# Performance work log

Hardware: AMD Instinct MI355X
Metric: run time of the kernel (lower is better)

## Reference

```python
import jax, jax.numpy as jnp
import numpy as np

HIDDEN = 1024
OUT = 16

def setup_inputs() -> dict:
    key = jax.random.key(0)
    ks = jax.random.split(key, 12)
    bs, hl, hf = 256, 256, 32
    T, ad = 64, 16
    flat = hl * hf
    s = lambda fi, fo: 1.0 / np.sqrt(fi)
    return {
        "history": jax.random.normal(ks[0], (bs, hl, hf), jnp.float32),
        "action": jax.random.normal(ks[1], (bs, T, ad), jnp.float32),
        # carry-init Dense layers (c and h)
        "Wc": jax.random.normal(ks[2], (flat, HIDDEN), jnp.float32) * s(flat, HIDDEN),
        "bc": jnp.zeros((HIDDEN,), jnp.float32),
        "Wh": jax.random.normal(ks[3], (flat, HIDDEN), jnp.float32) * s(flat, HIDDEN),
        "bh": jnp.zeros((HIDDEN,), jnp.float32),
        # LSTM cell: gates ordered [i, f, g, o]; input dense has no bias (flax LSTMCell)
        "Wi": jax.random.normal(ks[4], (ad, 4 * HIDDEN), jnp.float32) * s(ad, HIDDEN),
        "Wr": jax.random.normal(ks[5], (HIDDEN, 4 * HIDDEN), jnp.float32) * s(HIDDEN, HIDDEN),
        "bg": jnp.zeros((4 * HIDDEN,), jnp.float32),
        # output projection
        "Wo": jax.random.normal(ks[6], (HIDDEN, OUT), jnp.float32) * s(HIDDEN, OUT),
        "bo": jnp.zeros((OUT,), jnp.float32),
    }


def reference(history, action, Wc, bc, Wh, bh, Wi, Wr, bg, Wo, bo):
    bs = history.shape[0]
    flat = history.reshape(bs, -1)
    c0 = jax.nn.relu(flat @ Wc + bc)  # [bs, H]
    h0 = jax.nn.relu(flat @ Wh + bh)  # [bs, H]

    # precompute input contribution to gates for all steps: [T, bs, 4H]
    xg = jnp.einsum('bta,ag->tbg', action, Wi)

    def step(carry, xg_t):
        c, h = carry
        g = xg_t + h @ Wr + bg  # [bs, 4H]
        i, f, gg, o = jnp.split(g, 4, axis=-1)
        c = jax.nn.sigmoid(f) * c + jax.nn.sigmoid(i) * jnp.tanh(gg)
        h = jax.nn.sigmoid(o) * jnp.tanh(c)
        return (c, h), h

    _, hs = jax.lax.scan(step, (c0, h0), xg)  # hs: [T, bs, H]
    x = jnp.transpose(hs, (1, 0, 2))  # [bs, T, H]
    # Dropout is deterministic (identity)
    return x @ Wo + bo  # [bs, T, OUT]
```

## Files before the change

### kernel.cpp

```cpp
#include <hip/hip_runtime.h>
#include <math.h>

#define BS      256
#define FLAT    8192
#define H       1024
#define G4      4096
#define T_STEPS 64
#define AD      16
#define NOUT    16

typedef __attribute__((ext_vector_type(8))) short    bf16x8;
typedef __attribute__((ext_vector_type(4))) float    f32x4;
typedef __attribute__((ext_vector_type(8))) unsigned short u16x8;

__device__ __forceinline__ float sigf(float x) { return 1.0f / (1.0f + __expf(-x)); }
__device__ __forceinline__ float tanh_fast(float x) {
    float a = fabsf(x);
    float e = __expf(-2.0f * a);
    float r = (1.0f - e) / (1.0f + e);
    return copysignf(r, x);
}
__device__ __forceinline__ unsigned short f2bf(float x) {
    unsigned int u = __float_as_uint(x);
    unsigned int r = (u + 0x7FFFu + ((u >> 16) & 1u)) >> 16;
    return (unsigned short)r;
}

#define OFF_WRP  (1u<<20)
#define OFF_WIP  (OFF_WRP + (8u<<20))
#define OFF_BGP  (OFF_WIP + (256u<<10))
#define OFF_WOP  (OFF_BGP + (16u<<10))
#define OFF_BAR  (OFF_WOP + (32u<<10))
#define OFF_AXP  (10u<<20)
#define OFF_HALL (11u<<20)
#define OFF_AHP  (44u<<20)
#define OFF_PART (48u<<20)

#define HALL_STRIDE 262144u

__global__ __launch_bounds__(256) void pack_wr(const float* __restrict__ Wr,
                                               unsigned short* __restrict__ Wp)
{
    int g  = blockIdx.x * 256 + threadIdx.x;
    int l  = g & 63;
    int nt = (g >> 6) & 3;
    int kc = (g >> 8) & 31;
    int nb = g >> 13;
    int col   = nt * 1024 + nb * 16 + (l & 15);
    int kbase = kc * 32 + (l >> 4) * 8;
    u16x8 o;
    #pragma unroll
    for (int i = 0; i < 8; ++i)
        o[i] = f2bf(Wr[(size_t)(kbase + i) * G4 + col]);
    *(u16x8*)&Wp[(size_t)g * 8] = o;
}

__global__ __launch_bounds__(256) void pack_wi(const float* __restrict__ Wi,
                                               unsigned short* __restrict__ Wp)
{
    int g  = blockIdx.x * 256 + threadIdx.x;
    int l  = g & 63;
    int nt = (g >> 6) & 3;
    int nb = g >> 8;
    int col   = nt * 1024 + nb * 16 + (l & 15);
    int kbase = (l >> 4) * 8;
    u16x8 o;
    #pragma unroll
    for (int i = 0; i < 8; ++i)
        o[i] = (kbase + i < AD) ? f2bf(Wi[(size_t)(kbase + i) * G4 + col]) : (unsigned short)0;
    *(u16x8*)&Wp[(size_t)g * 8] = o;
}

__global__ __launch_bounds__(256) void pack_bg(const float* __restrict__ bg,
                                               float* __restrict__ bgp)
{
    int t = blockIdx.x * 256 + threadIdx.x;
    int jj = t & 15, nt = (t >> 4) & 3, nb = t >> 6;
    bgp[t] = bg[nt * 1024 + nb * 16 + jj];
}

__global__ __launch_bounds__(256) void pack_hist(const float* __restrict__ hist,
                                                 unsigned short* __restrict__ Ap)
{
    int g  = blockIdx.x * 256 + threadIdx.x;
    int l  = g & 63;
    int kc = (g >> 6) & 255;
    int mb = g >> 14;
    const float* src = hist + (size_t)(mb * 16 + (l & 15)) * FLAT + kc * 32 + (l >> 4) * 8;
    float4 v0 = *(const float4*)src;
    float4 v1 = *(const float4*)(src + 4);
    u16x8 o;
    o[0]=f2bf(v0.x); o[1]=f2bf(v0.y); o[2]=f2bf(v0.z); o[3]=f2bf(v0.w);
    o[4]=f2bf(v1.x); o[5]=f2bf(v1.y); o[6]=f2bf(v1.z); o[7]=f2bf(v1.w);
    *(u16x8*)&Ap[(size_t)g * 8] = o;
}

__global__ __launch_bounds__(256) void pack_wb(const float* __restrict__ Wc,
                                               const float* __restrict__ Wh,
                                               unsigned short* __restrict__ Bp)
{
    int g  = blockIdx.x * 256 + threadIdx.x;
    int l  = g & 63;
    int kc = (g >> 6) & 255;
    int nb = g >> 14;
    const float* src = (nb & 64) ? Wh : Wc;
    int n = (nb & 63) * 16 + (l & 15);
    int k = kc * 32 + (l >> 4) * 8;
    u16x8 o;
    #pragma unroll
    for (int i = 0; i < 8; ++i)
        o[i] = f2bf(src[(size_t)(k + i) * H + n]);
    *(u16x8*)&Bp[(size_t)g * 8] = o;
}

__global__ __launch_bounds__(256) void pack_act(const float* __restrict__ act,
                                                unsigned short* __restrict__ Axp)
{
    int g = blockIdx.x * 256 + threadIdx.x;
    int l = g & 63;
    int q = (g >> 6) & 15;
    int t = g >> 10;
    int row = q * 16 + (l & 15);
    int kb  = (l >> 4) * 8;
    u16x8 o;
    if (kb < AD) {
        const float* src = act + ((size_t)row * T_STEPS + t) * AD + kb;
        float4 v0 = *(const float4*)src;
        float4 v1 = *(const float4*)(src + 4);
        o[0]=f2bf(v0.x); o[1]=f2bf(v0.y); o[2]=f2bf(v0.z); o[3]=f2bf(v0.w);
        o[4]=f2bf(v1.x); o[5]=f2bf(v1.y); o[6]=f2bf(v1.z); o[7]=f2bf(v1.w);
    } else {
        o = (u16x8){0,0,0,0,0,0,0,0};
    }
    *(u16x8*)&Axp[(size_t)g * 8] = o;
}

__global__ __launch_bounds__(256) void pack_wo(const float* __restrict__ Wo,
                                               unsigned short* __restrict__ Wop)
{
    int g = blockIdx.x * 256 + threadIdx.x;
    int l = g & 63;
    int kc = g >> 6;
    u16x8 o;
    #pragma unroll
    for (int i = 0; i < 8; ++i)
        o[i] = f2bf(Wo[(size_t)(kc * 32 + (l >> 4) * 8 + i) * NOUT + (l & 15)]);
    *(u16x8*)&Wop[(size_t)g * 8] = o;
}

__global__ void bar_init(unsigned int* bar) {
    if (threadIdx.x == 0 && blockIdx.x == 0) *bar = 0u;
}

__global__ __launch_bounds__(256) void init_gemm_mfma(
    const unsigned short* __restrict__ Ap,
    const unsigned short* __restrict__ Bp,
    float* __restrict__ part)
{
    const int wg  = blockIdx.x;
    const int mb  = wg & 3;
    const int nbl = (wg >> 2) & 15;
    const int ks  = wg >> 6;
    const int tid = threadIdx.x;
    const int wv  = tid >> 6;
    const int l   = tid & 63;
    const int wm  = wv & 1;
    const int wn  = wv >> 1;

    const bf16x8* AV = (const bf16x8*)Ap;
    const bf16x8* BV = (const bf16x8*)Bp;
    const int am0 = mb * 4 + wm * 2;
    const int bn0 = nbl * 8 + wn * 4;
    const bf16x8* A0 = AV + (size_t)am0 * 16384 + l;
    const bf16x8* A1 = A0 + 16384;
    const bf16x8* B0 = BV + (size_t)bn0 * 16384 + l;
    const bf16x8* B1 = B0 + 16384;
    const bf16x8* B2 = B1 + 16384;
    const bf16x8* B3 = B2 + 16384;

    const int k0 = ks * 64;
    f32x4 acc[2][4];
    #pragma unroll
    for (int m = 0; m < 2; ++m)
        #pragma unroll
        for (int n = 0; n < 4; ++n)
            acc[m][n] = (f32x4){0.f, 0.f, 0.f, 0.f};

    bf16x8 a0 = A0[(size_t)k0 * 64], a1 = A1[(size_t)k0 * 64];
    bf16x8 b0 = B0[(size_t)k0 * 64], b1 = B1[(size_t)k0 * 64];
    bf16x8 b2 = B2[(size_t)k0 * 64], b3 = B3[(size_t)k0 * 64];

    for (int kc = k0; kc < k0 + 64; ++kc) {
        bf16x8 na0, na1, nb0, nb1, nb2, nb3;
        const bool more = (kc + 1) < k0 + 64;
        if (more) {
            size_t off = (size_t)(kc + 1) * 64;
            na0 = A0[off]; na1 = A1[off];
            nb0 = B0[off]; nb1 = B1[off]; nb2 = B2[off]; nb3 = B3[off];
        }
        acc[0][0] = __builtin_amdgcn_mfma_f32_16x16x32_bf16(a0, b0, acc[0][0], 0, 0, 0);
        acc[0][1] = __builtin_amdgcn_mfma_f32_16x16x32_bf16(a0, b1, acc[0][1], 0, 0, 0);
        acc[0][2] = __builtin_amdgcn_mfma_f32_16x16x32_bf16(a0, b2, acc[0][2], 0, 0, 0);
        acc[0][3] = __builtin_amdgcn_mfma_f32_16x16x32_bf16(a0, b3, acc[0][3], 0, 0, 0);
        acc[1][0] = __builtin_amdgcn_mfma_f32_16x16x32_bf16(a1, b0, acc[1][0], 0, 0, 0);
        acc[1][1] = __builtin_amdgcn_mfma_f32_16x16x32_bf16(a1, b1, acc[1][1], 0, 0, 0);
        acc[1][2] = __builtin_amdgcn_mfma_f32_16x16x32_bf16(a1, b2, acc[1][2], 0, 0, 0);
        acc[1][3] = __builtin_amdgcn_mfma_f32_16x16x32_bf16(a1, b3, acc[1][3], 0, 0, 0);
        if (more) { a0 = na0; a1 = na1; b0 = nb0; b1 = nb1; b2 = nb2; b3 = nb3; }
    }

    const int rbase = mb * 64 + wm * 32 + (l >> 4) * 4;
    const int cbase = nbl * 128 + wn * 64 + (l & 15);
    float* pdst = part + (size_t)ks * (BS * 2048);
    #pragma unroll
    for (int m = 0; m < 2; ++m)
        #pragma unroll
        for (int n = 0; n < 4; ++n)
            #pragma unroll
            for (int r = 0; r < 4; ++r)
                pdst[(size_t)(rbase + m * 16 + r) * 2048 + cbase + n * 16] = acc[m][n][r];
}

__global__ __launch_bounds__(256) void init_reduce(
    const float* __restrict__ part,
    const float* __restrict__ bc, const float* __restrict__ bh,
    float* __restrict__ cbuf, unsigned short* __restrict__ hp0)
{
    int e = blockIdx.x * 256 + threadIdx.x;
    int row = e >> 11, col = e & 2047;
    float s = (col < 1024) ? bc[col] : bh[col - 1024];
    #pragma unroll
    for (int ks = 0; ks < 4; ++ks)
        s += part[(size_t)ks * (BS * 2048) + e];
    s = fmaxf(s, 0.f);
    if (col < 1024) {
        cbuf[(size_t)row * H + col] = s;
    } else {
        int hid = col - 1024;
        int off = (row >> 6) * 65536 + (hid >> 5) * 2048 + ((row >> 4) & 3) * 512
                + ((((hid >> 3) & 3) << 4) + (row & 15)) * 8 + (hid & 7);
        hp0[off] = f2bf(s);
    }
}

__global__ __launch_bounds__(256) void lstm_scan_persist(
    const unsigned short* __restrict__ Axp,
    const unsigned short* __restrict__ Wip,
    const unsigned short* __restrict__ Wrp,
    const float* __restrict__ bgp,
    const float* __restrict__ cbuf,
    unsigned short* __restrict__ hall,
    unsigned int*   __restrict__ bar)
{
    __shared__ __align__(16) unsigned short sB[2][4096];

    const int tid = threadIdx.x;
    const int wg  = blockIdx.x;
    const int mb  = wg >> 6;
    const int nb  = wg & 63;
    const int wv  = tid >> 6;
    const int l   = tid & 63;

    const int jj   = l & 15;
    const int hid  = nb * 16 + jj;
    const int rowb = mb * 64 + wv * 16 + (l >> 4) * 4;
    const int kcp  = nb >> 1;
    const int hgrp = ((nb & 1) << 1) | (jj >> 3);
    const int ii   = jj & 7;
    const int pbase = mb * 65536 + kcp * 2048 + wv * 512 + hgrp * 128 + ii;

    float c_reg[4];
    #pragma unroll
    for (int r = 0; r < 4; ++r)
        c_reg[r] = cbuf[(size_t)(rowb + r) * H + hid];

    const bf16x8* WiB = ((const bf16x8*)Wip) + nb * 256;
    const bf16x8 wb0 = WiB[0 * 64 + l], wb1 = WiB[1 * 64 + l],
                 wb2 = WiB[2 * 64 + l], wb3 = WiB[3 * 64 + l];
    const float g0 = bgp[nb * 64 +  0 + jj];
    const float g1 = bgp[nb * 64 + 16 + jj];
    const float g2 = bgp[nb * 64 + 32 + jj];
    const float g3 = bgp[nb * 64 + 48 + jj];

    const u16x8* Bsrc = (const u16x8*)(Wrp + (size_t)nb * 65536);

    #pragma unroll 1
    for (int t = 0; t < T_STEPS; ++t) {
        const unsigned short* Ap = hall + (size_t)t * HALL_STRIDE;
        unsigned int* An32 = (unsigned int*)(hall + (size_t)(t + 1) * HALL_STRIDE);

        {
            u16x8 s0 = Bsrc[tid], s1 = Bsrc[256 + tid];
            *(u16x8*)&sB[0][tid * 8]         = s0;
            *(u16x8*)&sB[0][(256 + tid) * 8] = s1;
        }
        u16x8 stg0 = Bsrc[512 + tid];
        u16x8 stg1 = Bsrc[768 + tid];

        const bf16x8* Asrc = ((const bf16x8*)Ap) + mb * 8192 + wv * 64 + l;
        bf16x8 aE0 = Asrc[0],   aE1 = Asrc[256];
        bf16x8 aO0 = Asrc[512], aO1 = Asrc[768];

        f32x4 acc[4];
        acc[0] = (f32x4){ g0, g0, g0, g0 };
        acc[1] = (f32x4){ g1, g1, g1, g1 };
        acc[2] = (f32x4){ g2, g2, g2, g2 };
        acc[3] = (f32x4){ g3, g3, g3, g3 };
        {
            bf16x8 aa = *(((const bf16x8*)Axp) + ((size_t)t * 16 + mb * 4 + wv) * 64 + l);
            acc[0] = __builtin_amdgcn_mfma_f32_16x16x32_bf16(aa, wb0, acc[0], 0, 0, 0);
            acc[1] = __builtin_amdgcn_mfma_f32_16x16x32_bf16(aa, wb1, acc[1], 0, 0, 0);
            acc[2] = __builtin_amdgcn_mfma_f32_16x16x32_bf16(aa, wb2, acc[2], 0, 0, 0);
            acc[3] = __builtin_amdgcn_mfma_f32_16x16x32_bf16(aa, wb3, acc[3], 0, 0, 0);
        }
        __syncthreads();

        #define CHUNK_BODY(C, CB, AX0, AX1)                                             \
        {                                                                               \
            bf16x8 n0, n1;                                                              \
            if ((C) < 14) { n0 = Asrc[(2*(C)+4) * 256]; n1 = Asrc[(2*(C)+5) * 256]; }   \
            bf16x8 bf00 = *(const bf16x8*)&sB[CB][(0 * 64 + l) * 8];                    \
            bf16x8 bf01 = *(const bf16x8*)&sB[CB][(1 * 64 + l) * 8];                    \
            bf16x8 bf02 = *(const bf16x8*)&sB[CB][(2 * 64 + l) * 8];                    \
            bf16x8 bf03 = *(const bf16x8*)&sB[CB][(3 * 64 + l) * 8];                    \
            bf16x8 bf10 = *(const bf16x8*)&sB[CB][(4 * 64 + l) * 8];                    \
            bf16x8 bf11 = *(const bf16x8*)&sB[CB][(5 * 64 + l) * 8];                    \
            bf16x8 bf12 = *(const bf16x8*)&sB[CB][(6 * 64 + l) * 8];                    \
            bf16x8 bf13 = *(const bf16x8*)&sB[CB][(7 * 64 + l) * 8];                    \
            if ((C) < 15) {                                                             \
                *(u16x8*)&sB[(CB) ^ 1][tid * 8]         = stg0;                         \
                *(u16x8*)&sB[(CB) ^ 1][(256 + tid) * 8] = stg1;                         \
            }                                                                           \
            if ((C) < 14) {                                                             \
                stg0 = Bsrc[((C) + 2) * 512 + tid];                                     \
                stg1 = Bsrc[((C) + 2) * 512 + 256 + tid];                               \
            }                                                                           \
            acc[0] = __builtin_amdgcn_mfma_f32_16x16x32_bf16(AX0, bf00, acc[0], 0,0,0); \
            acc[1] = __builtin_amdgcn_mfma_f32_16x16x32_bf16(AX0, bf01, acc[1], 0,0,0); \
            acc[2] = __builtin_amdgcn_mfma_f32_16x16x32_bf16(AX0, bf02, acc[2], 0,0,0); \
            acc[3] = __builtin_amdgcn_mfma_f32_16x16x32_bf16(AX0, bf03, acc[3], 0,0,0); \
            acc[0] = __builtin_amdgcn_mfma_f32_16x16x32_bf16(AX1, bf10, acc[0], 0,0,0); \
            acc[1] = __builtin_amdgcn_mfma_f32_16x16x32_bf16(AX1, bf11, acc[1], 0,0,0); \
            acc[2] = __builtin_amdgcn_mfma_f32_16x16x32_bf16(AX1, bf12, acc[2], 0,0,0); \
            acc[3] = __builtin_amdgcn_mfma_f32_16x16x32_bf16(AX1, bf13, acc[3], 0,0,0); \
            if ((C) < 14) { AX0 = n0; AX1 = n1; }                                       \
            __syncthreads();                                                            \
        }

        for (int it = 0; it < 8; ++it) {
            const int c0 = 2 * it;
            CHUNK_BODY(c0,     0, aE0, aE1)
            CHUNK_BODY(c0 + 1, 1, aO0, aO1)
        }
        #undef CHUNK_BODY

        #pragma unroll
        for (int r = 0; r < 4; ++r) {
            float gi = acc[0][r], gf = acc[1][r], gg = acc[2][r], go = acc[3][r];
            float cv = sigf(gf) * c_reg[r] + sigf(gi) * tanh_fast(gg);
            c_reg[r] = cv;
            float hv = sigf(go) * tanh_fast(cv);
            unsigned int hb = (unsigned int)f2bf(hv);
            unsigned int pb = (unsigned int)__shfl_xor((int)hb, 1, 64) & 0xFFFFu;
            if ((jj & 1) == 0) {
                unsigned int val = (hb & 0xFFFFu) | (pb << 16);
                int poff = pbase + (((l >> 4) * 4 + r) << 3);
                __hip_atomic_store(&An32[poff >> 1], val,
                                   __ATOMIC_RELAXED, __HIP_MEMORY_SCOPE_AGENT);
            }
        }

        if (t < T_STEPS - 1) {
            __syncthreads();
            if (tid == 0) {
                __hip_atomic_fetch_add(bar, 1u, __ATOMIC_RELAXED,
                                       __HIP_MEMORY_SCOPE_AGENT);
                const unsigned int target = 256u * (unsigned int)(t + 1);
                while (__hip_atomic_load(bar, __ATOMIC_RELAXED,
                                         __HIP_MEMORY_SCOPE_AGENT) < target) {
                    __builtin_amdgcn_s_sleep(2);
                }
            }
            __syncthreads();
        }
    }
}

__global__ __launch_bounds__(256) void out_gemm(
    const unsigned short* __restrict__ hall,
    const unsigned short* __restrict__ Wop,
    const float* __restrict__ bo,
    float* __restrict__ out)
{
    __shared__ __align__(16) unsigned short sWo[32 * 64 * 8];
    const int tid = threadIdx.x;
    #pragma unroll
    for (int u = 0; u < 8; ++u) {
        int idx = u * 256 + tid;
        *(u16x8*)&sWo[idx * 8] = ((const u16x8*)Wop)[idx];
    }
    __syncthreads();

    const int wv  = tid >> 6;
    const int l   = tid & 63;
    const int gid = blockIdx.x * 4 + wv;
    const int t   = gid >> 4;
    const int rt  = gid & 15;

    const bf16x8* Asrc = ((const bf16x8*)(hall + (size_t)(t + 1) * HALL_STRIDE))
                       + (rt >> 2) * 8192 + (rt & 3) * 64 + l;

    f32x4 acc = (f32x4){0.f, 0.f, 0.f, 0.f};
    bf16x8 a = Asrc[0];
    for (int kc = 0; kc < 32; ++kc) {
        bf16x8 an;
        if (kc < 31) an = Asrc[(kc + 1) * 256];
        bf16x8 w = *(const bf16x8*)&sWo[(kc * 64 + l) * 8];
        acc = __builtin_amdgcn_mfma_f32_16x16x32_bf16(a, w, acc, 0, 0, 0);
        if (kc < 31) a = an;
    }

    const float bias = bo[l & 15];
    #pragma unroll
    for (int r = 0; r < 4; ++r) {
        int b = rt * 16 + (l >> 4) * 4 + r;
        out[((size_t)b * T_STEPS + t) * NOUT + (l & 15)] = acc[r] + bias;
    }
}

extern "C" void kernel_launch(void* const* d_in, const int* in_sizes, int n_in,
                              void* d_out, int out_size, void* d_ws, size_t ws_size,
                              hipStream_t stream)
{
    const float* hist = (const float*)d_in[0];
    const float* act  = (const float*)d_in[1];
    const float* Wc   = (const float*)d_in[2];
    const float* bc   = (const float*)d_in[3];
    const float* Wh   = (const float*)d_in[4];
    const float* bh   = (const float*)d_in[5];
    const float* Wi   = (const float*)d_in[6];
    const float* Wr   = (const float*)d_in[7];
    const float* bg   = (const float*)d_in[8];
    const float* Wo   = (const float*)d_in[9];
    const float* bo   = (const float*)d_in[10];
    float* out = (float*)d_out;

    char* W = (char*)d_ws;
    float*          cbuf = (float*)W;
    unsigned short* Wrp  = (unsigned short*)(W + OFF_WRP);
    unsigned short* Wip  = (unsigned short*)(W + OFF_WIP);
    float*          bgp  = (float*)(W + OFF_BGP);
    unsigned short* Wop  = (unsigned short*)(W + OFF_WOP);
    unsigned int*   bar  = (unsigned int*)(W + OFF_BAR);
    unsigned short* Axp  = (unsigned short*)(W + OFF_AXP);
    unsigned short* hall = (unsigned short*)(W + OFF_HALL);
    unsigned short* Bwp  = (unsigned short*)(W + OFF_HALL);
    unsigned short* Ahp  = (unsigned short*)(W + OFF_AHP);
    float*          part = (float*)(W + OFF_PART);

    bar_init <<<dim3(1),    dim3(64),  0, stream>>>(bar);
    pack_wr  <<<dim3(2048), dim3(256), 0, stream>>>(Wr, Wrp);
    pack_wi  <<<dim3(64),   dim3(256), 0, stream>>>(Wi, Wip);
    pack_bg  <<<dim3(16),   dim3(256), 0, stream>>>(bg, bgp);
    pack_hist<<<dim3(1024), dim3(256), 0, stream>>>(hist, Ahp);
    pack_wb  <<<dim3(8192), dim3(256), 0, stream>>>(Wc, Wh, Bwp);
    pack_act <<<dim3(256),  dim3(256), 0, stream>>>(act, Axp);
    pack_wo  <<<dim3(8),    dim3(256), 0, stream>>>(Wo, Wop);

    init_gemm_mfma<<<dim3(256), dim3(256), 0, stream>>>(Ahp, Bwp, part);
    init_reduce  <<<dim3(2048), dim3(256), 0, stream>>>(part, bc, bh, cbuf, hall);

    lstm_scan_persist<<<dim3(256), dim3(256), 0, stream>>>(
        Axp, Wip, Wrp, bgp, cbuf, hall, bar);

    out_gemm<<<dim3(256), dim3(256), 0, stream>>>(hall, Wop, bo, out);
}
```

Baseline: 718.3 us.

## Split recurrent GEMM K dimension across two wave groups per scan block

The persistent LSTM scan block grows from 256 to 512 threads. Two wave groups each handle half of the K range of h@Wr, each with its own double-buffered shared-memory staging of Wr, and their partial gate sums are combined through shared memory before the first group applies the cell update. All 16 A fragments of h are also loaded at the start of each step instead of being prefetched one chunk at a time. The goal is to shorten the serial per-step latency of the recurrence: half the chunks and half the block barriers per group per step. The cost is a shared-memory reduction, an extra barrier, more registers and more shared memory per block.

```diff
diff --git a/kernel.cpp b/kernel.cpp
--- a/kernel.cpp
+++ b/kernel.cpp
@@ -243,7 +243,7 @@
     }
 }
 
-__global__ __launch_bounds__(256) void lstm_scan_persist(
+__global__ __launch_bounds__(512) void lstm_scan_persist(
     const unsigned short* __restrict__ Axp,
     const unsigned short* __restrict__ Wip,
     const unsigned short* __restrict__ Wrp,
@@ -252,7 +252,8 @@
     unsigned short* __restrict__ hall,
     unsigned int*   __restrict__ bar)
 {
-    __shared__ __align__(16) unsigned short sB[2][4096];
+    __shared__ __align__(16) unsigned short sB[2][2][4096];
+    float* red = (float*)&sB[1][0][0];
 
     const int tid = threadIdx.x;
     const int wg  = blockIdx.x;
@@ -260,19 +261,24 @@
     const int nb  = wg & 63;
     const int wv  = tid >> 6;
     const int l   = tid & 63;
+    const int kg  = wv >> 2;
+    const int wq  = wv & 3;
+    const int gt  = tid & 255;
 
     const int jj   = l & 15;
     const int hid  = nb * 16 + jj;
-    const int rowb = mb * 64 + wv * 16 + (l >> 4) * 4;
+    const int rowb = mb * 64 + wq * 16 + (l >> 4) * 4;
     const int kcp  = nb >> 1;
     const int hgrp = ((nb & 1) << 1) | (jj >> 3);
     const int ii   = jj & 7;
-    const int pbase = mb * 65536 + kcp * 2048 + wv * 512 + hgrp * 128 + ii;
-
-    float c_reg[4];
-    #pragma unroll
-    for (int r = 0; r < 4; ++r)
-        c_reg[r] = cbuf[(size_t)(rowb + r) * H + hid];
+    const int pbase = mb * 65536 + kcp * 2048 + wq * 512 + hgrp * 128 + ii;
+
+    float c_reg[4] = {0.f, 0.f, 0.f, 0.f};
+    if (kg == 0) {
+        #pragma unroll
+        for (int r = 0; r < 4; ++r)
+            c_reg[r] = cbuf[(size_t)(rowb + r) * H + hid];
+    }
 
     const bf16x8* WiB = ((const bf16x8*)Wip) + nb * 256;
     const bf16x8 wb0 = WiB[0 * 64 + l], wb1 = WiB[1 * 64 + l],
@@ -282,7 +288,8 @@
     const float g2 = bgp[nb * 64 + 32 + jj];
     const float g3 = bgp[nb * 64 + 48 + jj];
 
-    const u16x8* Bsrc = (const u16x8*)(Wrp + (size_t)nb * 65536);
+    const u16x8* BsrcG = (const u16x8*)(Wrp + (size_t)nb * 65536) + (size_t)kg * 8 * 512;
+    unsigned short (*sBg)[4096] = sB[kg];
 
     #pragma unroll 1
     for (int t = 0; t < T_STEPS; ++t) {
@@ -290,83 +297,97 @@
         unsigned int* An32 = (unsigned int*)(hall + (size_t)(t + 1) * HALL_STRIDE);
 
         {
-            u16x8 s0 = Bsrc[tid], s1 = Bsrc[256 + tid];
-            *(u16x8*)&sB[0][tid * 8]         = s0;
-            *(u16x8*)&sB[0][(256 + tid) * 8] = s1;
-        }
-        u16x8 stg0 = Bsrc[512 + tid];
-        u16x8 stg1 = Bsrc[768 + tid];
-
-        const bf16x8* Asrc = ((const bf16x8*)Ap) + mb * 8192 + wv * 64 + l;
-        bf16x8 aE0 = Asrc[0],   aE1 = Asrc[256];
-        bf16x8 aO0 = Asrc[512], aO1 = Asrc[768];
+            u16x8 s0 = BsrcG[gt], s1 = BsrcG[256 + gt];
+            *(u16x8*)&sBg[0][gt * 8]         = s0;
+            *(u16x8*)&sBg[0][(256 + gt) * 8] = s1;
+        }
+        u16x8 stg0 = BsrcG[512 + gt];
+        u16x8 stg1 = BsrcG[768 + gt];
+
+        const bf16x8* Asrc = ((const bf16x8*)Ap) + mb * 8192 + wq * 64 + l;
+        bf16x8 af[16];
+        #pragma unroll
+        for (int q = 0; q < 16; ++q)
+            af[q] = Asrc[(size_t)(kg * 16 + q) * 256];
 
         f32x4 acc[4];
-        acc[0] = (f32x4){ g0, g0, g0, g0 };
-        acc[1] = (f32x4){ g1, g1, g1, g1 };
-        acc[2] = (f32x4){ g2, g2, g2, g2 };
-        acc[3] = (f32x4){ g3, g3, g3, g3 };
-        {
-            bf16x8 aa = *(((const bf16x8*)Axp) + ((size_t)t * 16 + mb * 4 + wv) * 64 + l);
+        if (kg == 0) {
+            acc[0] = (f32x4){ g0, g0, g0, g0 };
+            acc[1] = (f32x4){ g1, g1, g1, g1 };
+            acc[2] = (f32x4){ g2, g2, g2, g2 };
+            acc[3] = (f32x4){ g3, g3, g3, g3 };
+            bf16x8 aa = *(((const bf16x8*)Axp) + ((size_t)t * 16 + mb * 4 + wq) * 64 + l);
             acc[0] = __builtin_amdgcn_mfma_f32_16x16x32_bf16(aa, wb0, acc[0], 0, 0, 0);
             acc[1] = __builtin_amdgcn_mfma_f32_16x16x32_bf16(aa, wb1, acc[1], 0, 0, 0);
             acc[2] = __builtin_amdgcn_mfma_f32_16x16x32_bf16(aa, wb2, acc[2], 0, 0, 0);
             acc[3] = __builtin_amdgcn_mfma_f32_16x16x32_bf16(aa, wb3, acc[3], 0, 0, 0);
+        } else {
+            #pragma unroll
+            for (int n = 0; n < 4; ++n)
+                acc[n] = (f32x4){0.f, 0.f, 0.f, 0.f};
         }
         __syncthreads();
 
-        #define CHUNK_BODY(C, CB, AX0, AX1)                                             \
-        {                                                                               \
-            bf16x8 n0, n1;                                                              \
-            if ((C) < 14) { n0 = Asrc[(2*(C)+4) * 256]; n1 = Asrc[(2*(C)+5) * 256]; }   \
-            bf16x8 bf00 = *(const bf16x8*)&sB[CB][(0 * 64 + l) * 8];                    \
-            bf16x8 bf01 = *(const bf16x8*)&sB[CB][(1 * 64 + l) * 8];                    \
-            bf16x8 bf02 = *(const bf16x8*)&sB[CB][(2 * 64 + l) * 8];                    \
-            bf16x8 bf03 = *(const bf16x8*)&sB[CB][(3 * 64 + l) * 8];                    \
-            bf16x8 bf10 = *(const bf16x8*)&sB[CB][(4 * 64 + l) * 8];                    \
-            bf16x8 bf11 = *(const bf16x8*)&sB[CB][(5 * 64 + l) * 8];                    \
-            bf16x8 bf12 = *(const bf16x8*)&sB[CB][(6 * 64 + l) * 8];                    \
-            bf16x8 bf13 = *(const bf16x8*)&sB[CB][(7 * 64 + l) * 8];                    \
-            if ((C) < 15) {                                                             \
-                *(u16x8*)&sB[(CB) ^ 1][tid * 8]         = stg0;                         \
-                *(u16x8*)&sB[(CB) ^ 1][(256 + tid) * 8] = stg1;                         \
-            }                                                                           \
-            if ((C) < 14) {                                                             \
-                stg0 = Bsrc[((C) + 2) * 512 + tid];                                     \
-                stg1 = Bsrc[((C) + 2) * 512 + 256 + tid];                               \
-            }                                                                           \
-            acc[0] = __builtin_amdgcn_mfma_f32_16x16x32_bf16(AX0, bf00, acc[0], 0,0,0); \
-            acc[1] = __builtin_amdgcn_mfma_f32_16x16x32_bf16(AX0, bf01, acc[1], 0,0,0); \
-            acc[2] = __builtin_amdgcn_mfma_f32_16x16x32_bf16(AX0, bf02, acc[2], 0,0,0); \
-            acc[3] = __builtin_amdgcn_mfma_f32_16x16x32_bf16(AX0, bf03, acc[3], 0,0,0); \
-            acc[0] = __builtin_amdgcn_mfma_f32_16x16x32_bf16(AX1, bf10, acc[0], 0,0,0); \
-            acc[1] = __builtin_amdgcn_mfma_f32_16x16x32_bf16(AX1, bf11, acc[1], 0,0,0); \
-            acc[2] = __builtin_amdgcn_mfma_f32_16x16x32_bf16(AX1, bf12, acc[2], 0,0,0); \
-            acc[3] = __builtin_amdgcn_mfma_f32_16x16x32_bf16(AX1, bf13, acc[3], 0,0,0); \
-            if ((C) < 14) { AX0 = n0; AX1 = n1; }                                       \
-            __syncthreads();                                                            \
-        }
-
-        for (int it = 0; it < 8; ++it) {
-            const int c0 = 2 * it;
-            CHUNK_BODY(c0,     0, aE0, aE1)
-            CHUNK_BODY(c0 + 1, 1, aO0, aO1)
-        }
-        #undef CHUNK_BODY
-
         #pragma unroll
-        for (int r = 0; r < 4; ++r) {
-            float gi = acc[0][r], gf = acc[1][r], gg = acc[2][r], go = acc[3][r];
-            float cv = sigf(gf) * c_reg[r] + sigf(gi) * tanh_fast(gg);
-            c_reg[r] = cv;
-            float hv = sigf(go) * tanh_fast(cv);
-            unsigned int hb = (unsigned int)f2bf(hv);
-            unsigned int pb = (unsigned int)__shfl_xor((int)hb, 1, 64) & 0xFFFFu;
-            if ((jj & 1) == 0) {
-                unsigned int val = (hb & 0xFFFFu) | (pb << 16);
-                int poff = pbase + (((l >> 4) * 4 + r) << 3);
-                __hip_atomic_store(&An32[poff >> 1], val,
-                                   __ATOMIC_RELAXED, __HIP_MEMORY_SCOPE_AGENT);
+        for (int cc = 0; cc < 8; ++cc) {
+            const int cb = cc & 1;
+            bf16x8 bf00 = *(const bf16x8*)&sBg[cb][(0 * 64 + l) * 8];
+            bf16x8 bf01 = *(const bf16x8*)&sBg[cb][(1 * 64 + l) * 8];
+            bf16x8 bf02 = *(const bf16x8*)&sBg[cb][(2 * 64 + l) * 8];
+            bf16x8 bf03 = *(const bf16x8*)&sBg[cb][(3 * 64 + l) * 8];
+            bf16x8 bf10 = *(const bf16x8*)&sBg[cb][(4 * 64 + l) * 8];
+            bf16x8 bf11 = *(const bf16x8*)&sBg[cb][(5 * 64 + l) * 8];
+            bf16x8 bf12 = *(const bf16x8*)&sBg[cb][(6 * 64 + l) * 8];
+            bf16x8 bf13 = *(const bf16x8*)&sBg[cb][(7 * 64 + l) * 8];
+            if (cc < 7) {
+                *(u16x8*)&sBg[cb ^ 1][gt * 8]         = stg0;
+                *(u16x8*)&sBg[cb ^ 1][(256 + gt) * 8] = stg1;
+            }
+            if (cc < 6) {
+                stg0 = BsrcG[(cc + 2) * 512 + gt];
+                stg1 = BsrcG[(cc + 2) * 512 + 256 + gt];
+            }
+            acc[0] = __builtin_amdgcn_mfma_f32_16x16x32_bf16(af[2*cc],   bf00, acc[0], 0,0,0);
+            acc[1] = __builtin_amdgcn_mfma_f32_16x16x32_bf16(af[2*cc],   bf01, acc[1], 0,0,0);
+            acc[2] = __builtin_amdgcn_mfma_f32_16x16x32_bf16(af[2*cc],   bf02, acc[2], 0,0,0);
+            acc[3] = __builtin_amdgcn_mfma_f32_16x16x32_bf16(af[2*cc],   bf03, acc[3], 0,0,0);
+            acc[0] = __builtin_amdgcn_mfma_f32_16x16x32_bf16(af[2*cc+1], bf10, acc[0], 0,0,0);
+            acc[1] = __builtin_amdgcn_mfma_f32_16x16x32_bf16(af[2*cc+1], bf11, acc[1], 0,0,0);
+            acc[2] = __builtin_amdgcn_mfma_f32_16x16x32_bf16(af[2*cc+1], bf12, acc[2], 0,0,0);
+            acc[3] = __builtin_amdgcn_mfma_f32_16x16x32_bf16(af[2*cc+1], bf13, acc[3], 0,0,0);
+            __syncthreads();
+        }
+
+        if (kg == 1) {
+            #pragma unroll
+            for (int n = 0; n < 4; ++n)
+                #pragma unroll
+                for (int r = 0; r < 4; ++r)
+                    red[(n * 4 + r) * 256 + gt] = acc[n][r];
+        }
+        __syncthreads();
+
+        if (kg == 0) {
+            #pragma unroll
+            for (int n = 0; n < 4; ++n)
+                #pragma unroll
+                for (int r = 0; r < 4; ++r)
+                    acc[n][r] += red[(n * 4 + r) * 256 + gt];
+
+            #pragma unroll
+            for (int r = 0; r < 4; ++r) {
+                float gi = acc[0][r], gf = acc[1][r], gg = acc[2][r], go = acc[3][r];
+                float cv = sigf(gf) * c_reg[r] + sigf(gi) * tanh_fast(gg);
+                c_reg[r] = cv;
+                float hv = sigf(go) * tanh_fast(cv);
+                unsigned int hb = (unsigned int)f2bf(hv);
+                unsigned int pb = (unsigned int)__shfl_xor((int)hb, 1, 64) & 0xFFFFu;
+                if ((jj & 1) == 0) {
+                    unsigned int val = (hb & 0xFFFFu) | (pb << 16);
+                    int poff = pbase + (((l >> 4) * 4 + r) << 3);
+                    __hip_atomic_store(&An32[poff >> 1], val,
+                                       __ATOMIC_RELAXED, __HIP_MEMORY_SCOPE_AGENT);
+                }
             }
         }
 
@@ -470,7 +491,7 @@
     init_gemm_mfma<<<dim3(256), dim3(256), 0, stream>>>(Ahp, Bwp, part);
     init_reduce  <<<dim3(2048), dim3(256), 0, stream>>>(part, bc, bh, cbuf, hall);
 
-    lstm_scan_persist<<<dim3(256), dim3(256), 0, stream>>>(
+    lstm_scan_persist<<<dim3(256), dim3(512), 0, stream>>>(
         Axp, Wip, Wrp, bgp, cbuf, hall, bar);
 
     out_gemm<<<dim3(256), dim3(256), 0, stream>>>(hall, Wop, bo, out);
```

Measured after the change: 728.4 us. About the same (+1.4%).
